# Kernel optimization log

Hardware: AMD Instinct MI355X
Metric: run time of the kernel (lower is better)

The kernel has to match this reference:

```python
import jax, jax.numpy as jnp
import numpy as np


def setup_inputs() -> dict:
    key = jax.random.key(0)
    k1, k2, k3, k4 = jax.random.split(key, 4)
    B, S, H, D = 4, 2048, 1024, 1024
    X = jax.random.normal(k1, (B, S, H), dtype=jnp.float32)
    # nn.Linear weight stored as [out, in]; we store as [in, out] for x @ W
    scale = 1.0 / np.sqrt(H)
    Wq = jax.random.normal(k2, (H, D), dtype=jnp.float32) * scale
    Wk = jax.random.normal(k3, (H, D), dtype=jnp.float32) * scale
    Wv = jax.random.normal(k4, (H, D), dtype=jnp.float32) * scale
    return {"X": X, "Wq": Wq, "Wk": Wk, "Wv": Wv}


def reference(X, Wq, Wk, Wv):
    B, S, H = X.shape
    q = X @ Wq  # [B, S, D]
    k = X @ Wk
    v = X @ Wv
    D = k.shape[-1]
    scores = jnp.einsum('bqd,bkd->bqk', q, k) / jnp.sqrt(jnp.float32(D))
    causal = jnp.tril(jnp.ones((S, S), dtype=bool))  # block_size mask sliced to S
    scores = jnp.where(causal, scores, -jnp.inf)
    weights = jax.nn.softmax(scores, axis=-1)  # dropout p=0.0 -> identity
    return jnp.einsum('bqk,bkd->bqd', weights, v)
```

## Files before the change

### kernel.cpp

```cpp
#include <hip/hip_runtime.h>

#define AS1 __attribute__((address_space(1)))
#define AS3 __attribute__((address_space(3)))

typedef __attribute__((ext_vector_type(8))) short short8;
typedef __attribute__((ext_vector_type(4))) float floatx4;

__device__ __forceinline__ short f2bf(float f) {
  union { float f; unsigned u; } v; v.f = f;
  return (short)((v.u + 0x7fffu + ((v.u >> 16) & 1u)) >> 16);
}
__device__ __forceinline__ float bf2f(short s) {
  union { unsigned u; float f; } v; v.u = ((unsigned)(unsigned short)s) << 16;
  return v.f;
}

__device__ __forceinline__ void gload_lds16(const void* g, void* l) {
  __builtin_amdgcn_global_load_lds((const AS1 unsigned*)g, (AS3 unsigned*)l, 16, 0, 0);
}

__device__ __forceinline__ void stage128x64(const short* __restrict__ G, long rowBase, long ld,
                                            int kBase, short* lds, int lane, int wave) {
  const short* gb = G + rowBase * ld + (long)kBase + (long)(lane >> 3) * ld + (lane & 7) * 8;
#pragma unroll
  for (int j = 0; j < 4; ++j) {
    int c = wave * 4 + j;
    gload_lds16(gb + (long)c * 8 * ld, lds + c * 512);
  }
}

__device__ __forceinline__ void mfma_step(const short* lA, const short* lB, floatx4 acc[4][4],
                                          int lane, int wm, int wn) {
#pragma unroll
  for (int kk = 0; kk < 64; kk += 32) {
    short8 a[4], b[4];
    int kq = kk + (lane >> 4) * 8;
#pragma unroll
    for (int i = 0; i < 4; ++i) {
      a[i] = *(const short8*)(lA + (wm * 64 + i * 16 + (lane & 15)) * 64 + kq);
      b[i] = *(const short8*)(lB + (wn * 64 + i * 16 + (lane & 15)) * 64 + kq);
    }
#pragma unroll
    for (int i = 0; i < 4; ++i)
#pragma unroll
      for (int j = 0; j < 4; ++j)
        acc[i][j] = __builtin_amdgcn_mfma_f32_16x16x32_bf16(a[i], b[j], acc[i][j], 0, 0, 0);
  }
}

__global__ void prep_inputs(const float* __restrict__ X, const float* __restrict__ Wq,
                            const float* __restrict__ Wk, const float* __restrict__ Wv,
                            short* __restrict__ Xb, short* __restrict__ Wt) {
  __shared__ float t[32][33];
  if (blockIdx.x < 8192) {
    long i = ((long)blockIdx.x * 256 + threadIdx.x) * 4;
    float4 v = *(const float4*)(X + i);
    short4 o;
    o.x = f2bf(v.x); o.y = f2bf(v.y); o.z = f2bf(v.z); o.w = f2bf(v.w);
    *(short4*)(Xb + i) = o;
  } else {
    int idx = blockIdx.x - 8192;
    int z = idx >> 10, rem = idx & 1023;
    int bx = rem >> 5, by = rem & 31;
    const float* W = z == 0 ? Wq : (z == 1 ? Wk : Wv);
    short* O = Wt + (long)z * 1024 * 1024;
    int tx = threadIdx.x & 31, ty = threadIdx.x >> 5;
    int x = bx * 32 + tx;
    int y0 = by * 32;
    for (int j = ty; j < 32; j += 8)
      t[j][tx] = W[(long)(y0 + j) * 1024 + x];
    __syncthreads();
    int x2 = by * 32 + tx;
    int y2 = bx * 32;
    for (int j = ty; j < 32; j += 8)
      O[(long)(y2 + j) * 1024 + x2] = f2bf(t[tx][j]);
  }
}

__global__ __launch_bounds__(256, 3) void gemm_qkv(const short* __restrict__ Xb,
                                                   const short* __restrict__ Wt,
                                                   short* __restrict__ Q, short* __restrict__ K2,
                                                   short* __restrict__ Vt) {
  __shared__ short lA[128 * 64], lB[128 * 64];
  const int lane = threadIdx.x & 63, wave = threadIdx.x >> 6;
  const int wm = wave >> 1, wn = wave & 1;
  const int z = blockIdx.z;
  const short* Bm = Wt + (long)z * 1024 * 1024;
  const long mBase = (long)blockIdx.x * 128;
  const long nBase = (long)blockIdx.y * 128;

  floatx4 acc[4][4];
  const floatx4 zero = {0.f, 0.f, 0.f, 0.f};
#pragma unroll
  for (int i = 0; i < 4; ++i)
#pragma unroll
    for (int j = 0; j < 4; ++j) acc[i][j] = zero;

  for (int kt = 0; kt < 16; ++kt) {
    stage128x64(Xb, mBase, 1024, kt * 64, lA, lane, wave);
    stage128x64(Bm, nBase, 1024, kt * 64, lB, lane, wave);
    __syncthreads();
    mfma_step(lA, lB, acc, lane, wm, wn);
    __syncthreads();
  }

  if (z < 2) {
    short* out = (z == 0) ? Q : K2;
#pragma unroll
    for (int i = 0; i < 4; ++i)
#pragma unroll
      for (int j = 0; j < 4; ++j) {
        int col = (int)nBase + wn * 64 + j * 16 + (lane & 15);
#pragma unroll
        for (int r = 0; r < 4; ++r) {
          long m = mBase + wm * 64 + i * 16 + (lane >> 4) * 4 + r;
          out[m * 1024 + col] = f2bf(acc[i][j][r]);
        }
      }
  } else {
    const long bb = mBase >> 11;
    const int sBase = (int)(mBase & 2047);
#pragma unroll
    for (int i = 0; i < 4; ++i) {
      int s0 = sBase + wm * 64 + i * 16 + ((lane >> 4) << 2);
#pragma unroll
      for (int j = 0; j < 4; ++j) {
        int col = (int)nBase + wn * 64 + j * 16 + (lane & 15);
        short4 o;
        o.x = f2bf(acc[i][j][0]); o.y = f2bf(acc[i][j][1]);
        o.z = f2bf(acc[i][j][2]); o.w = f2bf(acc[i][j][3]);
        *(short4*)(Vt + ((bb * 1024 + col) * 2048 + s0)) = o;
      }
    }
  }
}

__global__ __launch_bounds__(256, 3) void scores_exp(const short* __restrict__ Q,
                                                     const short* __restrict__ Kk,
                                                     short* __restrict__ E, float* __restrict__ l) {
  __shared__ short lA[128 * 64], lB[128 * 64];
  const int lane = threadIdx.x & 63, wave = threadIdx.x >> 6;
  const int wm = wave >> 1, wn = wave & 1;
  const int b = blockIdx.y;
  int qt = 0, rem = blockIdx.x;
  while (rem > qt) { rem -= (qt + 1); ++qt; }
  const int kt = rem;

  const long rowQ = (long)b * 2048 + (long)qt * 128;
  const long rowK = (long)b * 2048 + (long)kt * 128;

  floatx4 acc[4][4];
  const floatx4 zero = {0.f, 0.f, 0.f, 0.f};
#pragma unroll
  for (int i = 0; i < 4; ++i)
#pragma unroll
    for (int j = 0; j < 4; ++j) acc[i][j] = zero;

  for (int it = 0; it < 16; ++it) {
    stage128x64(Q, rowQ, 1024, it * 64, lA, lane, wave);
    stage128x64(Kk, rowK, 1024, it * 64, lB, lane, wave);
    __syncthreads();
    mfma_step(lA, lB, acc, lane, wm, wn);
    __syncthreads();
  }

  short* Eb = E + (long)b * 2048 * 2048;
  float* lrow = l + (long)b * 2048;
#pragma unroll
  for (int i = 0; i < 4; ++i) {
#pragma unroll
    for (int r = 0; r < 4; ++r) {
      int ri = wm * 64 + i * 16 + (lane >> 4) * 4 + r;
      int qrow = qt * 128 + ri;
      float p = 0.f;
#pragma unroll
      for (int j = 0; j < 4; ++j) {
        int col = kt * 128 + wn * 64 + j * 16 + (lane & 15);
        float s = acc[i][j][r] * 0.03125f;
        float e = (col <= qrow) ? __expf(s) : 0.0f;
        short eb = f2bf(e);
        Eb[(long)qrow * 2048 + col] = eb;
        p += bf2f(eb);
      }
      for (int m = 1; m < 16; m <<= 1) p += __shfl_xor(p, m, 64);
      if ((lane & 15) == 0) atomicAdd(&lrow[qrow], p);
    }
  }
}

__global__ __launch_bounds__(256, 3) void pv_gemm(const short* __restrict__ E,
                                                  const short* __restrict__ Vt,
                                                  const float* __restrict__ l,
                                                  float* __restrict__ part,
                                                  float* __restrict__ out) {
  __shared__ short lA[128 * 64], lB[128 * 64];
  const int lane = threadIdx.x & 63, wave = threadIdx.x >> 6;
  const int wm = wave >> 1, wn = wave & 1;
  const int x = blockIdx.x, dt = blockIdx.y, b = blockIdx.z;

  int qt, it0, it1, mode;
  if (x < 16) {
    qt = 8 + (x >> 1);
    const int T = (qt + 1) * 2, c0 = T >> 1;
    if ((x & 1) == 0) { it0 = 0; it1 = c0; mode = 1; }
    else              { it0 = c0; it1 = T; mode = 2; }
  } else {
    qt = x - 16; it0 = 0; it1 = (qt + 1) * 2; mode = 0;
  }

  const short* Eb = E + (long)b * 2048 * 2048;
  const short* Vb = Vt + (long)b * 1024 * 2048;
  const float* lrow = l + (long)b * 2048;

  floatx4 acc[4][4];
  const floatx4 zero = {0.f, 0.f, 0.f, 0.f};
#pragma unroll
  for (int i = 0; i < 4; ++i)
#pragma unroll
    for (int j = 0; j < 4; ++j) acc[i][j] = zero;

  for (int it = it0; it < it1; ++it) {
    stage128x64(Eb, (long)qt * 128, 2048, it * 64, lA, lane, wave);
    stage128x64(Vb, (long)dt * 128, 2048, it * 64, lB, lane, wave);
    __syncthreads();
    mfma_step(lA, lB, acc, lane, wm, wn);
    __syncthreads();
  }

  if (mode == 2) {
    float* P = part + ((((long)b * 8 + (qt - 8)) * 8 + dt) << 14);
#pragma unroll
    for (int i = 0; i < 4; ++i)
#pragma unroll
      for (int r = 0; r < 4; ++r) {
        int ri = wm * 64 + i * 16 + (lane >> 4) * 4 + r;
#pragma unroll
        for (int j = 0; j < 4; ++j) {
          int ci = wn * 64 + j * 16 + (lane & 15);
          P[ri * 128 + ci] = acc[i][j][r];
        }
      }
  } else {
#pragma unroll
    for (int i = 0; i < 4; ++i)
#pragma unroll
      for (int r = 0; r < 4; ++r) {
        int qrow = qt * 128 + wm * 64 + i * 16 + (lane >> 4) * 4 + r;
        float scale = (mode == 0) ? 1.0f / lrow[qrow] : 1.0f;
#pragma unroll
        for (int j = 0; j < 4; ++j) {
          int d = dt * 128 + wn * 64 + j * 16 + (lane & 15);
          out[((long)b * 2048 + qrow) * 1024 + d] = acc[i][j][r] * scale;
        }
      }
  }
}

__global__ void pv_reduce(float* __restrict__ out, const float* __restrict__ part,
                          const float* __restrict__ l) {
  const int idx = blockIdx.x;
  const int b = idx >> 10;
  const int row = 1024 + (idx & 1023);
  const int t = threadIdx.x;
  const int dt = t >> 5, dl = (t << 2) & 127;
  const float inv = 1.0f / l[((long)b << 11) + row];
  const long pbase = ((((long)b * 8 + ((row >> 7) - 8)) * 8 + dt) << 14) + ((row & 127) << 7) + dl;
  const long obase = (((long)b * 2048 + row) << 10) + (t << 2);
  float4 o = *(const float4*)(out + obase);
  float4 p = *(const float4*)(part + pbase);
  o.x = (o.x + p.x) * inv; o.y = (o.y + p.y) * inv;
  o.z = (o.z + p.z) * inv; o.w = (o.w + p.w) * inv;
  *(float4*)(out + obase) = o;
}

extern "C" void kernel_launch(void* const* d_in, const int* in_sizes, int n_in,
                              void* d_out, int out_size, void* d_ws, size_t ws_size,
                              hipStream_t stream) {
  const float* X  = (const float*)d_in[0];
  const float* Wq = (const float*)d_in[1];
  const float* Wk = (const float*)d_in[2];
  const float* Wv = (const float*)d_in[3];

  char* ws = (char*)d_ws;
  short* Xb = (short*)(ws);
  short* Wt = (short*)(ws + 16777216L);
  short* Q  = (short*)(ws + 23068672L);
  short* K2 = (short*)(ws + 39845888L);
  short* Vt = (short*)(ws + 56623104L);
  short* E  = (short*)(ws + 73400320L);
  float* l  = (float*)(ws + 106954752L);
  float* part = (float*)(ws);

  hipMemsetAsync(l, 0, 4 * 2048 * sizeof(float), stream);
  prep_inputs<<<11264, 256, 0, stream>>>(X, Wq, Wk, Wv, Xb, Wt);
  gemm_qkv<<<dim3(64, 8, 3), 256, 0, stream>>>(Xb, Wt, Q, K2, Vt);
  scores_exp<<<dim3(136, 4), 256, 0, stream>>>(Q, K2, E, l);
  pv_gemm<<<dim3(24, 8, 4), 256, 0, stream>>>(E, Vt, l, part, (float*)d_out);
  pv_reduce<<<4096, 256, 0, stream>>>((float*)d_out, part, l);
}
```

Baseline: 244.1 us.

## Stage exp scores through swizzled LDS and remap tiles for XCD locality

The scores_exp epilogue now writes the bf16 exp tile into XOR-swizzled shared memory and then stores it to global memory as coalesced 16-byte vectors, replacing scattered 2-byte stores. Its block index is also remapped so that each group of blocks (blockIdx mod 8, presumably one per XCD) handles 4x4 super-tiles of the causal triangle, which should improve L2 reuse of Q and K. The grid grows to 160 blocks and the surplus ones exit early. pv_gemm is remapped the same way, so blocks sharing a dt and pairing long and short qt rows land together, which is meant to improve cache locality and load balance.

```diff
diff --git a/kernel.cpp b/kernel.cpp
--- a/kernel.cpp
+++ b/kernel.cpp
@@ -138,13 +138,35 @@
 __global__ __launch_bounds__(256, 3) void scores_exp(const short* __restrict__ Q,
                                                      const short* __restrict__ Kk,
                                                      short* __restrict__ E, float* __restrict__ l) {
-  __shared__ short lA[128 * 64], lB[128 * 64];
+  __shared__ short lbuf[16384];
+  short* lA = lbuf;
+  short* lB = lbuf + 8192;
   const int lane = threadIdx.x & 63, wave = threadIdx.x >> 6;
   const int wm = wave >> 1, wn = wave & 1;
   const int b = blockIdx.y;
-  int qt = 0, rem = blockIdx.x;
-  while (rem > qt) { rem -= (qt + 1); ++qt; }
-  const int kt = rem;
+
+  const int r = blockIdx.x & 7, w = blockIdx.x >> 3;
+  int s, p;
+  if (r < 6) {
+    if (w >= 16) return;
+    s = (r == 5) ? 8 : r + 1 + ((r + 1) >> 1);
+    p = w;
+  } else {
+    if (w >= 20) return;
+    if (r == 6) s = (w < 10) ? 0 : 2;
+    else        s = (w < 10) ? 5 : 9;
+    p = (w < 10) ? w : w - 10;
+  }
+  const int QT = (s >= 1) + (s >= 3) + (s >= 6);
+  const int KT = s - (QT * (QT + 1)) / 2;
+  int dq, dk;
+  if (QT > KT) { dq = p >> 2; dk = p & 3; }
+  else {
+    dq = 0;
+    while ((dq + 1) * (dq + 2) / 2 <= p) ++dq;
+    dk = p - (dq * (dq + 1)) / 2;
+  }
+  const int qt = QT * 4 + dq, kt = KT * 4 + dk;
 
   const long rowQ = (long)b * 2048 + (long)qt * 128;
   const long rowK = (long)b * 2048 + (long)kt * 128;
@@ -164,27 +186,38 @@
     __syncthreads();
   }
 
-  short* Eb = E + (long)b * 2048 * 2048;
   float* lrow = l + (long)b * 2048;
 #pragma unroll
   for (int i = 0; i < 4; ++i) {
 #pragma unroll
-    for (int r = 0; r < 4; ++r) {
-      int ri = wm * 64 + i * 16 + (lane >> 4) * 4 + r;
+    for (int rr = 0; rr < 4; ++rr) {
+      int ri = wm * 64 + i * 16 + (lane >> 4) * 4 + rr;
       int qrow = qt * 128 + ri;
-      float p = 0.f;
+      float psum = 0.f;
 #pragma unroll
       for (int j = 0; j < 4; ++j) {
-        int col = kt * 128 + wn * 64 + j * 16 + (lane & 15);
-        float s = acc[i][j][r] * 0.03125f;
-        float e = (col <= qrow) ? __expf(s) : 0.0f;
+        int ci = wn * 64 + j * 16 + (lane & 15);
+        int col = kt * 128 + ci;
+        float sc = acc[i][j][rr] * 0.03125f;
+        float e = (col <= qrow) ? __expf(sc) : 0.0f;
         short eb = f2bf(e);
-        Eb[(long)qrow * 2048 + col] = eb;
-        p += bf2f(eb);
-      }
-      for (int m = 1; m < 16; m <<= 1) p += __shfl_xor(p, m, 64);
-      if ((lane & 15) == 0) atomicAdd(&lrow[qrow], p);
+        lbuf[ri * 128 + ((((ci >> 3) ^ (ri & 15)) << 3) | (ci & 7))] = eb;
+        psum += bf2f(eb);
+      }
+      for (int m = 1; m < 16; m <<= 1) psum += __shfl_xor(psum, m, 64);
+      if ((lane & 15) == 0) atomicAdd(&lrow[qrow], psum);
     }
+  }
+  __syncthreads();
+
+  short* Eb = E + (long)b * 4194304;
+  const long ebase = (long)(qt * 128) * 2048 + kt * 128;
+#pragma unroll
+  for (int pp = 0; pp < 8; ++pp) {
+    int g = pp * 256 + threadIdx.x;
+    int row = g >> 4, c = g & 15;
+    short8 v = *(const short8*)(lbuf + row * 128 + ((c ^ (row & 15)) << 3));
+    *(short8*)(Eb + ebase + (long)row * 2048 + c * 8) = v;
   }
 }
 
@@ -196,16 +229,20 @@
   __shared__ short lA[128 * 64], lB[128 * 64];
   const int lane = threadIdx.x & 63, wave = threadIdx.x >> 6;
   const int wm = wave >> 1, wn = wave & 1;
-  const int x = blockIdx.x, dt = blockIdx.y, b = blockIdx.z;
+  const int xx = blockIdx.x;
+  const int dt = xx / 24;
+  const int within = xx % 24;
+  const int r = within & 7, wsel = within >> 3;
+  const int b = blockIdx.y;
 
   int qt, it0, it1, mode;
-  if (x < 16) {
-    qt = 8 + (x >> 1);
+  if (wsel == 2) {
+    qt = r; it0 = 0; it1 = (qt + 1) * 2; mode = 0;
+  } else {
+    qt = 15 - r;
     const int T = (qt + 1) * 2, c0 = T >> 1;
-    if ((x & 1) == 0) { it0 = 0; it1 = c0; mode = 1; }
-    else              { it0 = c0; it1 = T; mode = 2; }
-  } else {
-    qt = x - 16; it0 = 0; it1 = (qt + 1) * 2; mode = 0;
+    if (wsel == 0) { it0 = 0;  it1 = c0; mode = 1; }
+    else           { it0 = c0; it1 = T;  mode = 2; }
   }
 
   const short* Eb = E + (long)b * 2048 * 2048;
@@ -232,25 +269,25 @@
 #pragma unroll
     for (int i = 0; i < 4; ++i)
 #pragma unroll
-      for (int r = 0; r < 4; ++r) {
-        int ri = wm * 64 + i * 16 + (lane >> 4) * 4 + r;
+      for (int rr = 0; rr < 4; ++rr) {
+        int ri = wm * 64 + i * 16 + (lane >> 4) * 4 + rr;
 #pragma unroll
         for (int j = 0; j < 4; ++j) {
           int ci = wn * 64 + j * 16 + (lane & 15);
-          P[ri * 128 + ci] = acc[i][j][r];
+          P[ri * 128 + ci] = acc[i][j][rr];
         }
       }
   } else {
 #pragma unroll
     for (int i = 0; i < 4; ++i)
 #pragma unroll
-      for (int r = 0; r < 4; ++r) {
-        int qrow = qt * 128 + wm * 64 + i * 16 + (lane >> 4) * 4 + r;
+      for (int rr = 0; rr < 4; ++rr) {
+        int qrow = qt * 128 + wm * 64 + i * 16 + (lane >> 4) * 4 + rr;
         float scale = (mode == 0) ? 1.0f / lrow[qrow] : 1.0f;
 #pragma unroll
         for (int j = 0; j < 4; ++j) {
           int d = dt * 128 + wn * 64 + j * 16 + (lane & 15);
-          out[((long)b * 2048 + qrow) * 1024 + d] = acc[i][j][r] * scale;
+          out[((long)b * 2048 + qrow) * 1024 + d] = acc[i][j][rr] * scale;
         }
       }
   }
@@ -294,7 +331,7 @@
   hipMemsetAsync(l, 0, 4 * 2048 * sizeof(float), stream);
   prep_inputs<<<11264, 256, 0, stream>>>(X, Wq, Wk, Wv, Xb, Wt);
   gemm_qkv<<<dim3(64, 8, 3), 256, 0, stream>>>(Xb, Wt, Q, K2, Vt);
-  scores_exp<<<dim3(136, 4), 256, 0, stream>>>(Q, K2, E, l);
-  pv_gemm<<<dim3(24, 8, 4), 256, 0, stream>>>(E, Vt, l, part, (float*)d_out);
+  scores_exp<<<dim3(160, 4), 256, 0, stream>>>(Q, K2, E, l);
+  pv_gemm<<<dim3(192, 4), 256, 0, stream>>>(E, Vt, l, part, (float*)d_out);
   pv_reduce<<<4096, 256, 0, stream>>>((float*)d_out, part, l);
 }
```

Result: faster. 238.9 us (-2.1%).
